# Kernel optimization log

Measured on AMD Instinct MI355X. Metric: run time of the kernel, lower is better.

Reference implementation:

```python
import jax, jax.numpy as jnp
import numpy as np


def setup_inputs() -> dict:
    key = jax.random.key(0)
    k1, k2, k3, k4 = jax.random.split(key, 4)
    B, T, M, Din, Dout = 32, 24, 512, 64, 64
    x = jax.random.normal(k1, (B, T, M, Din), dtype=jnp.float32)
    adj = jax.random.uniform(k2, (M, M), dtype=jnp.float32)
    adj = adj / jnp.sum(adj, axis=-1, keepdims=True)  # row-normalized adjacency
    route_weights = jax.random.normal(k3, (M, Din, Dout), dtype=jnp.float32) * 0.05
    route_bias = jax.random.normal(k4, (M, 1, Dout), dtype=jnp.float32) * 0.05
    return {"x": x, "adj": adj, "route_weights": route_weights, "route_bias": route_bias}


def reference(x, adj, route_weights, route_bias):
    B, T, M, _ = x.shape
    xf = x.reshape(B * T, M, -1)                      # [BT, M, Din]
    # shared adjacency applied across all B*T graphs: one contraction instead of
    # a broadcast bmm
    h = jnp.einsum('mn,bnd->bmd', adj, xf)            # [BT, M, Din]
    # per-node (per-route) weight transform + per-route bias
    h = jnp.einsum('bmd,mdl->bml', h, route_weights)  # [BT, M, Dout]
    h = h + route_bias[:, 0, :][None, :, :]           # bias per route m
    return h.reshape(B, T, M, -1)
```

## Files before the change

### kernel.cpp

```cpp
#include <hip/hip_runtime.h>
#include <stdint.h>

typedef short bf16x8 __attribute__((ext_vector_type(8)));
typedef unsigned short u16x8 __attribute__((ext_vector_type(8)));
typedef float f32x4 __attribute__((ext_vector_type(4)));
typedef float f32x8 __attribute__((ext_vector_type(8)));

constexpr int BT_TOT = 768;
constexpr int M_N    = 512;
constexpr int DD     = 64;
constexpr int WROW   = 72;

__device__ __forceinline__ unsigned short f2bf(float f) {
  unsigned u = __builtin_bit_cast(unsigned, f);
  u += 0x7fffu + ((u >> 16) & 1u);
  return (unsigned short)(u >> 16);
}
__device__ __forceinline__ unsigned pk2(float a, float b) {
  return (unsigned)f2bf(a) | ((unsigned)f2bf(b) << 16);
}

__global__ __launch_bounds__(256)
void prep_adj(const float* __restrict__ adjg, unsigned short* __restrict__ wsadj) {
  int i = (blockIdx.x * 256 + threadIdx.x) * 8;
  f32x8 a = *(const f32x8*)(adjg + i);
  u16x8 r;
  #pragma unroll
  for (int j = 0; j < 8; ++j) r[j] = f2bf(a[j]);
  *(u16x8*)(wsadj + i) = r;
}

template<bool WS>
__global__ __launch_bounds__(256, 4)
void gconv_h(const float* __restrict__ xg,
             const float* __restrict__ adjf,
             const unsigned short* __restrict__ adjb,
             char* __restrict__ hout)
{
  __shared__ __align__(16) char xlds[2][8192];

  const int wid  = blockIdx.x;
  const int xcd  = wid & 7;
  const int slot = wid >> 3;
  const int mb   = slot & 3;
  const int bt   = (slot >> 2) * 8 + xcd;

  const int tid  = threadIdx.x;
  const int lane = tid & 63;
  const int wv   = tid >> 6;
  const int l15  = lane & 15;
  const int gg   = lane >> 4;
  const int c4   = l15;

  const float* xsrc = xg + (size_t)bt * (M_N * DD);

  f32x4 xv[4];
  auto load_x = [&](int c) {
    #pragma unroll
    for (int s = 0; s < 4; ++s) {
      const int n4 = s*4 + wv;
      xv[s] = *(const f32x4*)(xsrc + (size_t)(c*64 + n4*4 + gg) * DD + c4*4);
    }
  };
  auto write_x = [&](int c) {
    char* xt = &xlds[c & 1][0];
    const int d = c4*4 + gg;
    #pragma unroll
    for (int s = 0; s < 4; ++s) {
      const int n4 = s*4 + wv;
      unsigned u0 = pk2(xv[s].x, xv[s].y);
      unsigned u1 = pk2(xv[s].z, xv[s].w);
      unsigned t0 = __shfl_xor(u0, 32);
      unsigned t1 = __shfl_xor(u1, 32);
      unsigned v0 = (gg & 2) ? t1 : u0;
      unsigned v1 = (gg & 2) ? u1 : t0;
      unsigned s0 = __shfl_xor(v0, 16);
      unsigned s1 = __shfl_xor(v1, 16);
      unsigned F0 = (gg & 1) ? ((s0 >> 16) | (v0 & 0xFFFF0000u))
                             : ((v0 & 0xFFFFu) | (s0 << 16));
      unsigned F1 = (gg & 1) ? ((s1 >> 16) | (v1 & 0xFFFF0000u))
                             : ((v1 & 0xFFFFu) | (s1 << 16));
      uint2 o2; o2.x = F0; o2.y = F1;
      *(uint2*)(xt + d*128 + (((n4 >> 1) ^ (d & 7)) * 16) + (n4 & 1)*8) = o2;
    }
  };

  f32x4 acc[2][4];
  #pragma unroll
  for (int mt = 0; mt < 2; ++mt)
    #pragma unroll
    for (int dt = 0; dt < 4; ++dt) acc[mt][dt] = f32x4{0.f,0.f,0.f,0.f};

  load_x(0);
  write_x(0);
  __syncthreads();

  #pragma unroll
  for (int c = 0; c < 8; ++c) {
    u16x8 afr[2][2];
    if (WS) {
      #pragma unroll
      for (int kl = 0; kl < 2; ++kl)
        #pragma unroll
        for (int mt = 0; mt < 2; ++mt) {
          const int m = mb*128 + wv*32 + mt*16 + l15;
          afr[kl][mt] = *(const u16x8*)(adjb + (size_t)m*M_N + c*64 + kl*32 + gg*8);
        }
    } else {
      #pragma unroll
      for (int kl = 0; kl < 2; ++kl)
        #pragma unroll
        for (int mt = 0; mt < 2; ++mt) {
          const int m = mb*128 + wv*32 + mt*16 + l15;
          f32x8 a = *(const f32x8*)(adjf + (size_t)m*M_N + c*64 + kl*32 + gg*8);
          u16x8 r;
          #pragma unroll
          for (int j = 0; j < 8; ++j) r[j] = f2bf(a[j]);
          afr[kl][mt] = r;
        }
    }

    if (c < 7) load_x(c + 1);

    const char* xt = &xlds[c & 1][0];
    #pragma unroll
    for (int kl = 0; kl < 2; ++kl) {
      bf16x8 bfx[4];
      #pragma unroll
      for (int dt = 0; dt < 4; ++dt)
        bfx[dt] = __builtin_bit_cast(bf16x8,
            *(const u16x8*)(xt + (dt*16 + l15)*128 + ((kl*4 + gg) ^ (l15 & 7))*16));
      #pragma unroll
      for (int mt = 0; mt < 2; ++mt)
        #pragma unroll
        for (int dt = 0; dt < 4; ++dt)
          acc[mt][dt] = __builtin_amdgcn_mfma_f32_16x16x32_bf16(
              __builtin_bit_cast(bf16x8, afr[kl][mt]), bfx[dt], acc[mt][dt], 0,0,0);
    }

    if (c < 7) { write_x(c + 1); __syncthreads(); }
  }

  #pragma unroll
  for (int mt = 0; mt < 2; ++mt)
    #pragma unroll
    for (int dt = 0; dt < 4; ++dt)
      #pragma unroll
      for (int r = 0; r < 4; ++r) {
        int m = mb*128 + wv*32 + mt*16 + gg*4 + r;
        int d = dt*16 + l15;
        *(unsigned short*)(hout + ((size_t)bt*M_N + m)*256 + 2*d)
            = f2bf(acc[mt][dt][r]);
      }
}

__global__ __launch_bounds__(256, 4)
void route_mm(const char* __restrict__ hin,
              const float* __restrict__ wgt,
              const float* __restrict__ bias,
              float* __restrict__ outg)
{
  __shared__ unsigned short wb[128 * WROW];

  const int m0    = blockIdx.x * 2;
  const int btblk = blockIdx.y * 64;
  const int tid   = threadIdx.x;
  const int lane  = tid & 63;
  const int wv    = tid >> 6;
  const int l15   = lane & 15;
  const int gg    = lane >> 4;
  const int dp    = tid & 31;
  const int lo    = tid >> 5;

  { const float* q = wgt + ((size_t)m0*64 + dp*2)*64 + lo*8;
    f32x8 w0 = *(const f32x8*)q;          f32x8 w1 = *(const f32x8*)(q+64);
    f32x8 w2 = *(const f32x8*)(q+4096);   f32x8 w3 = *(const f32x8*)(q+4160);
    #pragma unroll
    for (int e = 0; e < 8; ++e) {
      int lrow = lo*8 + e;
      unsigned v0 = pk2(w0[e], w1[e]);
      unsigned v1 = pk2(w2[e], w3[e]);
      *(unsigned*)(wb + lrow*WROW + dp*2)        = v0;
      *(unsigned*)(wb + (64 + lrow)*WROW + dp*2) = v1;
    }
  }
  __syncthreads();

  const int btw0 = btblk + wv*16;

  #pragma unroll
  for (int mm = 0; mm < 2; ++mm) {
    const int m = m0 + mm;
    bf16x8 afr[2];
    #pragma unroll
    for (int ks = 0; ks < 2; ++ks) {
      const char* hp = hin + ((size_t)(btw0 + l15)*M_N + m)*256 + ks*64 + gg*16;
      afr[ks] = __builtin_bit_cast(bf16x8, *(const u16x8*)hp);
    }
    f32x4 acc[4];
    #pragma unroll
    for (int lt = 0; lt < 4; ++lt) acc[lt] = f32x4{0.f,0.f,0.f,0.f};
    #pragma unroll
    for (int lt = 0; lt < 4; ++lt)
      #pragma unroll
      for (int ks = 0; ks < 2; ++ks) {
        bf16x8 bfr = __builtin_bit_cast(bf16x8,
            *(const u16x8*)(wb + (mm*64 + lt*16 + l15)*WROW + ks*32 + gg*8));
        acc[lt] = __builtin_amdgcn_mfma_f32_16x16x32_bf16(afr[ks], bfr, acc[lt], 0,0,0);
      }
    #pragma unroll
    for (int lt = 0; lt < 4; ++lt) {
      float bv = bias[m*64 + lt*16 + l15];
      #pragma unroll
      for (int r = 0; r < 4; ++r) {
        size_t row = (size_t)(btw0 + gg*4 + r)*M_N + m;
        outg[row*64 + lt*16 + l15] = acc[lt][r] + bv;
      }
    }
  }
}

extern "C" void kernel_launch(void* const* d_in, const int* in_sizes, int n_in,
                              void* d_out, int out_size, void* d_ws, size_t ws_size,
                              hipStream_t stream) {
  const float* xg   = (const float*)d_in[0];
  const float* adjg = (const float*)d_in[1];
  const float* wgt  = (const float*)d_in[2];
  const float* bg   = (const float*)d_in[3];

  const size_t adj_bf_bytes = (size_t)M_N * M_N * 2;
  if (ws_size >= adj_bf_bytes) {
    unsigned short* wsadj = (unsigned short*)d_ws;
    prep_adj<<<dim3(M_N * M_N / (256 * 8)), dim3(256), 0, stream>>>(adjg, wsadj);
    gconv_h<true><<<dim3(3072), dim3(256), 0, stream>>>(
        xg, adjg, wsadj, (char*)d_out);
  } else {
    gconv_h<false><<<dim3(3072), dim3(256), 0, stream>>>(
        xg, adjg, nullptr, (char*)d_out);
  }
  route_mm<<<dim3(M_N/2, BT_TOT/64), dim3(256), 0, stream>>>(
      (const char*)d_out, wgt, bg, (float*)d_out);
}
```

Before: 107.2 us.

## Prefetch x two chunks ahead, change LDS swizzle, use lighter barriers

The gconv_h kernel now keeps two register buffers of x chunks, so global loads are issued two iterations ahead instead of one. The LDS XOR swizzle folds in higher row bits to reduce bank conflicts on the MFMA B-fragment reads. __syncthreads is replaced with an explicit lgkmcnt wait plus s_barrier, which avoids waiting on outstanding global loads at each barrier. This costs more VGPRs per thread, which could hurt occupancy under the 4-blocks-per-SIMD launch bound.

New measurement: 118.6 us. +10.6%, slower.

```diff
diff --git a/kernel.cpp b/kernel.cpp
--- a/kernel.cpp
+++ b/kernel.cpp
@@ -54,22 +54,23 @@
 
   const float* xsrc = xg + (size_t)bt * (M_N * DD);
 
-  f32x4 xv[4];
-  auto load_x = [&](int c) {
+  f32x4 xv[2][4];
+  auto load_x = [&](int c, int rb) {
     #pragma unroll
     for (int s = 0; s < 4; ++s) {
       const int n4 = s*4 + wv;
-      xv[s] = *(const f32x4*)(xsrc + (size_t)(c*64 + n4*4 + gg) * DD + c4*4);
+      xv[rb][s] = *(const f32x4*)(xsrc + (size_t)(c*64 + n4*4 + gg) * DD + c4*4);
     }
   };
-  auto write_x = [&](int c) {
+  auto write_x = [&](int c, int rb) {
     char* xt = &xlds[c & 1][0];
-    const int d = c4*4 + gg;
+    const int d   = c4*4 + gg;
+    const int g3d = (d & 7) ^ ((d >> 3) & 7);
     #pragma unroll
     for (int s = 0; s < 4; ++s) {
       const int n4 = s*4 + wv;
-      unsigned u0 = pk2(xv[s].x, xv[s].y);
-      unsigned u1 = pk2(xv[s].z, xv[s].w);
+      unsigned u0 = pk2(xv[rb][s].x, xv[rb][s].y);
+      unsigned u1 = pk2(xv[rb][s].z, xv[rb][s].w);
       unsigned t0 = __shfl_xor(u0, 32);
       unsigned t1 = __shfl_xor(u1, 32);
       unsigned v0 = (gg & 2) ? t1 : u0;
@@ -81,7 +82,7 @@
       unsigned F1 = (gg & 1) ? ((s1 >> 16) | (v1 & 0xFFFF0000u))
                              : ((v1 & 0xFFFFu) | (s1 << 16));
       uint2 o2; o2.x = F0; o2.y = F1;
-      *(uint2*)(xt + d*128 + (((n4 >> 1) ^ (d & 7)) * 16) + (n4 & 1)*8) = o2;
+      *(uint2*)(xt + d*128 + (((n4 >> 1) ^ g3d) * 16) + (n4 & 1)*8) = o2;
     }
   };
 
@@ -91,45 +92,44 @@
     #pragma unroll
     for (int dt = 0; dt < 4; ++dt) acc[mt][dt] = f32x4{0.f,0.f,0.f,0.f};
 
-  load_x(0);
-  write_x(0);
-  __syncthreads();
+  load_x(0, 0);
+  load_x(1, 1);
+  write_x(0, 0);
+  asm volatile("s_waitcnt lgkmcnt(0)" ::: "memory");
+  __builtin_amdgcn_s_barrier();
 
   #pragma unroll
   for (int c = 0; c < 8; ++c) {
     u16x8 afr[2][2];
-    if (WS) {
-      #pragma unroll
-      for (int kl = 0; kl < 2; ++kl)
-        #pragma unroll
-        for (int mt = 0; mt < 2; ++mt) {
-          const int m = mb*128 + wv*32 + mt*16 + l15;
+    #pragma unroll
+    for (int kl = 0; kl < 2; ++kl)
+      #pragma unroll
+      for (int mt = 0; mt < 2; ++mt) {
+        const int m = mb*128 + wv*32 + mt*16 + l15;
+        if (WS) {
           afr[kl][mt] = *(const u16x8*)(adjb + (size_t)m*M_N + c*64 + kl*32 + gg*8);
-        }
-    } else {
-      #pragma unroll
-      for (int kl = 0; kl < 2; ++kl)
-        #pragma unroll
-        for (int mt = 0; mt < 2; ++mt) {
-          const int m = mb*128 + wv*32 + mt*16 + l15;
+        } else {
           f32x8 a = *(const f32x8*)(adjf + (size_t)m*M_N + c*64 + kl*32 + gg*8);
           u16x8 r;
           #pragma unroll
           for (int j = 0; j < 8; ++j) r[j] = f2bf(a[j]);
           afr[kl][mt] = r;
         }
-    }
-
-    if (c < 7) load_x(c + 1);
+      }
+
+    if (c < 6) load_x(c + 2, c & 1);
 
     const char* xt = &xlds[c & 1][0];
     #pragma unroll
     for (int kl = 0; kl < 2; ++kl) {
       bf16x8 bfx[4];
       #pragma unroll
-      for (int dt = 0; dt < 4; ++dt)
+      for (int dt = 0; dt < 4; ++dt) {
+        const int row = dt*16 + l15;
+        const int g3r = (row & 7) ^ ((row >> 3) & 7);
         bfx[dt] = __builtin_bit_cast(bf16x8,
-            *(const u16x8*)(xt + (dt*16 + l15)*128 + ((kl*4 + gg) ^ (l15 & 7))*16));
+            *(const u16x8*)(xt + row*128 + (((kl*4 + gg) ^ g3r)) * 16));
+      }
       #pragma unroll
       for (int mt = 0; mt < 2; ++mt)
         #pragma unroll
@@ -138,7 +138,11 @@
               __builtin_bit_cast(bf16x8, afr[kl][mt]), bfx[dt], acc[mt][dt], 0,0,0);
     }
 
-    if (c < 7) { write_x(c + 1); __syncthreads(); }
+    if (c < 7) {
+      write_x(c + 1, (c + 1) & 1);
+      asm volatile("s_waitcnt lgkmcnt(0)" ::: "memory");
+      __builtin_amdgcn_s_barrier();
+    }
   }
 
   #pragma unroll
```

## Pre-transpose x to bf16 in a separate pass and batch two graphs per gconv block

Applied to the files above, without the earlier changes.

Adds a prep_x kernel that converts x to bf16 in a transposed, MFMA-friendly layout. It stores the result in the unused upper half of each output row. gconv_h then reads its B fragments straight from global memory with no LDS staging or barriers, and each block handles two bt slices, which halves the grid. The goal is to remove the repeated fp32 load, convert and shuffle work that each of the four m-blocks did per graph, and to reuse each adjacency fragment across two graphs. The cost is an extra kernel launch and an extra round trip of x through memory, plus more accumulator registers (launch bounds lowered to 3).

Result: slower. 169.9 us (+58.5%).

```diff
diff --git a/kernel.cpp b/kernel.cpp
--- a/kernel.cpp
+++ b/kernel.cpp
@@ -10,6 +10,7 @@
 constexpr int M_N    = 512;
 constexpr int DD     = 64;
 constexpr int WROW   = 72;
+
 
 __device__ __forceinline__ unsigned short f2bf(float f) {
   unsigned u = __builtin_bit_cast(unsigned, f);
@@ -30,128 +31,147 @@
   *(u16x8*)(wsadj + i) = r;
 }
 
+__global__ __launch_bounds__(256, 4)
+void prep_x(const float* __restrict__ xg, char* __restrict__ xout) {
+  __shared__ __align__(16) char lds[2][8192];
+
+  const int wid  = blockIdx.x;
+  const int bt   = wid >> 1;
+  const int half = wid & 1;
+  const int tid  = threadIdx.x;
+  const int lane = tid & 63;
+  const int wv   = tid >> 6;
+  const int gg   = lane >> 4;
+  const int c4   = lane & 15;
+
+  const float* xb = xg + (size_t)bt * (M_N * DD);
+
+  f32x4 xv[4];
+  auto load_c = [&](int c) {
+    #pragma unroll
+    for (int s = 0; s < 4; ++s)
+      xv[s] = *(const f32x4*)(xb + (size_t)(c*64 + s*16 + wv*4 + gg) * DD + c4*4);
+  };
+
+  load_c(half*4);
+  #pragma unroll
+  for (int cc = 0; cc < 4; ++cc) {
+    const int c = half*4 + cc;
+    char* xt = &lds[cc & 1][0];
+    {
+      const int d   = c4*4 + gg;
+      const int g3d = (d & 7) ^ ((d >> 3) & 7);
+      #pragma unroll
+      for (int s = 0; s < 4; ++s) {
+        const int n4 = s*4 + wv;
+        unsigned u0 = pk2(xv[s].x, xv[s].y);
+        unsigned u1 = pk2(xv[s].z, xv[s].w);
+        unsigned t0 = __shfl_xor(u0, 32);
+        unsigned t1 = __shfl_xor(u1, 32);
+        unsigned v0 = (gg & 2) ? t1 : u0;
+        unsigned v1 = (gg & 2) ? u1 : t0;
+        unsigned s0 = __shfl_xor(v0, 16);
+        unsigned s1 = __shfl_xor(v1, 16);
+        unsigned F0 = (gg & 1) ? ((s0 >> 16) | (v0 & 0xFFFF0000u))
+                               : ((v0 & 0xFFFFu) | (s0 << 16));
+        unsigned F1 = (gg & 1) ? ((s1 >> 16) | (v1 & 0xFFFF0000u))
+                               : ((v1 & 0xFFFFu) | (s1 << 16));
+        uint2 o2; o2.x = F0; o2.y = F1;
+        *(uint2*)(xt + d*128 + (((n4 >> 1) ^ g3d) * 16) + (n4 & 1)*8) = o2;
+      }
+    }
+    if (cc < 3) load_c(c + 1);
+    __syncthreads();
+    #pragma unroll
+    for (int h = 0; h < 2; ++h) {
+      const int g   = tid + h*256;
+      const int d   = g >> 3;
+      const int o   = g & 7;
+      const int g3d = (d & 7) ^ ((d >> 3) & 7);
+      u16x8 val = *(const u16x8*)(xt + d*128 + ((o ^ g3d) * 16));
+      *(u16x8*)(xout + ((size_t)(bt*512 + 8*d + c)) * 256 + 128 + o*16) = val;
+    }
+  }
+}
+
 template<bool WS>
-__global__ __launch_bounds__(256, 4)
-void gconv_h(const float* __restrict__ xg,
-             const float* __restrict__ adjf,
+__global__ __launch_bounds__(256, 3)
+void gconv_h(const float* __restrict__ adjf,
              const unsigned short* __restrict__ adjb,
-             char* __restrict__ hout)
+             char* __restrict__ dio)
 {
-  __shared__ __align__(16) char xlds[2][8192];
-
   const int wid  = blockIdx.x;
   const int xcd  = wid & 7;
   const int slot = wid >> 3;
   const int mb   = slot & 3;
-  const int bt   = (slot >> 2) * 8 + xcd;
+  const int btp  = (slot >> 2) * 8 + xcd;
+  const int bt0  = btp * 2;
 
   const int tid  = threadIdx.x;
   const int lane = tid & 63;
   const int wv   = tid >> 6;
   const int l15  = lane & 15;
   const int gg   = lane >> 4;
-  const int c4   = l15;
-
-  const float* xsrc = xg + (size_t)bt * (M_N * DD);
-
-  f32x4 xv[4];
-  auto load_x = [&](int c) {
-    #pragma unroll
-    for (int s = 0; s < 4; ++s) {
-      const int n4 = s*4 + wv;
-      xv[s] = *(const f32x4*)(xsrc + (size_t)(c*64 + n4*4 + gg) * DD + c4*4);
-    }
-  };
-  auto write_x = [&](int c) {
-    char* xt = &xlds[c & 1][0];
-    const int d = c4*4 + gg;
-    #pragma unroll
-    for (int s = 0; s < 4; ++s) {
-      const int n4 = s*4 + wv;
-      unsigned u0 = pk2(xv[s].x, xv[s].y);
-      unsigned u1 = pk2(xv[s].z, xv[s].w);
-      unsigned t0 = __shfl_xor(u0, 32);
-      unsigned t1 = __shfl_xor(u1, 32);
-      unsigned v0 = (gg & 2) ? t1 : u0;
-      unsigned v1 = (gg & 2) ? u1 : t0;
-      unsigned s0 = __shfl_xor(v0, 16);
-      unsigned s1 = __shfl_xor(v1, 16);
-      unsigned F0 = (gg & 1) ? ((s0 >> 16) | (v0 & 0xFFFF0000u))
-                             : ((v0 & 0xFFFFu) | (s0 << 16));
-      unsigned F1 = (gg & 1) ? ((s1 >> 16) | (v1 & 0xFFFF0000u))
-                             : ((v1 & 0xFFFFu) | (s1 << 16));
-      uint2 o2; o2.x = F0; o2.y = F1;
-      *(uint2*)(xt + d*128 + (((n4 >> 1) ^ (d & 7)) * 16) + (n4 & 1)*8) = o2;
-    }
-  };
-
-  f32x4 acc[2][4];
-  #pragma unroll
-  for (int mt = 0; mt < 2; ++mt)
-    #pragma unroll
-    for (int dt = 0; dt < 4; ++dt) acc[mt][dt] = f32x4{0.f,0.f,0.f,0.f};
-
-  load_x(0);
-  write_x(0);
-  __syncthreads();
-
-  #pragma unroll
-  for (int c = 0; c < 8; ++c) {
-    u16x8 afr[2][2];
-    if (WS) {
-      #pragma unroll
-      for (int kl = 0; kl < 2; ++kl)
+  const int mrow = mb*128 + wv*32;
+
+  f32x4 acc[2][2][4];
+  #pragma unroll
+  for (int bb = 0; bb < 2; ++bb)
+    #pragma unroll
+    for (int mt = 0; mt < 2; ++mt)
+      #pragma unroll
+      for (int dt = 0; dt < 4; ++dt) acc[bb][mt][dt] = f32x4{0.f,0.f,0.f,0.f};
+
+  #pragma unroll 4
+  for (int kl = 0; kl < 16; ++kl) {
+    bf16x8 afr[2];
+    #pragma unroll
+    for (int mt = 0; mt < 2; ++mt) {
+      const int m = mrow + mt*16 + l15;
+      if (WS) {
+        afr[mt] = __builtin_bit_cast(bf16x8,
+            *(const u16x8*)(adjb + (size_t)m*M_N + kl*32 + gg*8));
+      } else {
+        f32x8 a = *(const f32x8*)(adjf + (size_t)m*M_N + kl*32 + gg*8);
+        u16x8 r;
         #pragma unroll
-        for (int mt = 0; mt < 2; ++mt) {
-          const int m = mb*128 + wv*32 + mt*16 + l15;
-          afr[kl][mt] = *(const u16x8*)(adjb + (size_t)m*M_N + c*64 + kl*32 + gg*8);
-        }
-    } else {
-      #pragma unroll
-      for (int kl = 0; kl < 2; ++kl)
-        #pragma unroll
-        for (int mt = 0; mt < 2; ++mt) {
-          const int m = mb*128 + wv*32 + mt*16 + l15;
-          f32x8 a = *(const f32x8*)(adjf + (size_t)m*M_N + c*64 + kl*32 + gg*8);
-          u16x8 r;
-          #pragma unroll
-          for (int j = 0; j < 8; ++j) r[j] = f2bf(a[j]);
-          afr[kl][mt] = r;
-        }
-    }
-
-    if (c < 7) load_x(c + 1);
-
-    const char* xt = &xlds[c & 1][0];
-    #pragma unroll
-    for (int kl = 0; kl < 2; ++kl) {
-      bf16x8 bfx[4];
-      #pragma unroll
-      for (int dt = 0; dt < 4; ++dt)
-        bfx[dt] = __builtin_bit_cast(bf16x8,
-            *(const u16x8*)(xt + (dt*16 + l15)*128 + ((kl*4 + gg) ^ (l15 & 7))*16));
+        for (int j = 0; j < 8; ++j) r[j] = f2bf(a[j]);
+        afr[mt] = __builtin_bit_cast(bf16x8, r);
+      }
+    }
+    bf16x8 bfx[2][4];
+    #pragma unroll
+    for (int bb = 0; bb < 2; ++bb)
+      #pragma unroll
+      for (int dt = 0; dt < 4; ++dt) {
+        const int d = dt*16 + l15;
+        bfx[bb][dt] = __builtin_bit_cast(bf16x8, *(const u16x8*)(dio
+            + ((size_t)((bt0+bb)*512 + 8*d + (kl >> 1))) * 256
+            + 128 + (kl & 1)*64 + gg*16));
+      }
+    #pragma unroll
+    for (int bb = 0; bb < 2; ++bb)
       #pragma unroll
       for (int mt = 0; mt < 2; ++mt)
         #pragma unroll
         for (int dt = 0; dt < 4; ++dt)
-          acc[mt][dt] = __builtin_amdgcn_mfma_f32_16x16x32_bf16(
-              __builtin_bit_cast(bf16x8, afr[kl][mt]), bfx[dt], acc[mt][dt], 0,0,0);
-    }
-
-    if (c < 7) { write_x(c + 1); __syncthreads(); }
-  }
-
-  #pragma unroll
-  for (int mt = 0; mt < 2; ++mt)
-    #pragma unroll
-    for (int dt = 0; dt < 4; ++dt)
-      #pragma unroll
-      for (int r = 0; r < 4; ++r) {
-        int m = mb*128 + wv*32 + mt*16 + gg*4 + r;
-        int d = dt*16 + l15;
-        *(unsigned short*)(hout + ((size_t)bt*M_N + m)*256 + 2*d)
-            = f2bf(acc[mt][dt][r]);
-      }
+          acc[bb][mt][dt] = __builtin_amdgcn_mfma_f32_16x16x32_bf16(
+              afr[mt], bfx[bb][dt], acc[bb][mt][dt], 0,0,0);
+  }
+
+  #pragma unroll
+  for (int bb = 0; bb < 2; ++bb)
+    #pragma unroll
+    for (int mt = 0; mt < 2; ++mt)
+      #pragma unroll
+      for (int dt = 0; dt < 4; ++dt)
+        #pragma unroll
+        for (int r = 0; r < 4; ++r) {
+          const int m = mrow + mt*16 + gg*4 + r;
+          const int d = dt*16 + l15;
+          *(unsigned short*)(dio + ((size_t)(bt0+bb)*M_N + m)*256 + 2*d)
+              = f2bf(acc[bb][mt][dt][r]);
+        }
 }
 
 __global__ __launch_bounds__(256, 4)
@@ -228,15 +248,15 @@
   const float* wgt  = (const float*)d_in[2];
   const float* bg   = (const float*)d_in[3];
 
+  prep_x<<<dim3(BT_TOT * 2), dim3(256), 0, stream>>>(xg, (char*)d_out);
+
   const size_t adj_bf_bytes = (size_t)M_N * M_N * 2;
   if (ws_size >= adj_bf_bytes) {
     unsigned short* wsadj = (unsigned short*)d_ws;
     prep_adj<<<dim3(M_N * M_N / (256 * 8)), dim3(256), 0, stream>>>(adjg, wsadj);
-    gconv_h<true><<<dim3(3072), dim3(256), 0, stream>>>(
-        xg, adjg, wsadj, (char*)d_out);
+    gconv_h<true><<<dim3(1536), dim3(256), 0, stream>>>(adjg, wsadj, (char*)d_out);
   } else {
-    gconv_h<false><<<dim3(3072), dim3(256), 0, stream>>>(
-        xg, adjg, nullptr, (char*)d_out);
+    gconv_h<false><<<dim3(1536), dim3(256), 0, stream>>>(adjg, nullptr, (char*)d_out);
   }
   route_mm<<<dim3(M_N/2, BT_TOT/64), dim3(256), 0, stream>>>(
       (const char*)d_out, wgt, bg, (float*)d_out);
```
